# Optimization experiments

Measured on AMD Instinct MI355X. Metric: run time of the kernel, lower is better.

Reference implementation:

```python
import jax, jax.numpy as jnp
import numpy as np

B, TIN, TOUT = 128, 512, 64
IN_F, OUT_F, H = 64, 32, 1024
DEC_IN = IN_F + OUT_F  # decoder GRU input size


def setup_inputs() -> dict:
    key = jax.random.key(0)
    ks = jax.random.split(key, 24)
    s = 1.0 / np.sqrt(H)
    u = lambda k, shp: jax.random.uniform(k, shp, jnp.float32, -s, s)
    return {
        "enc_input": jax.random.normal(ks[0], (B, TIN, IN_F), jnp.float32),
        "dec_input": jax.random.normal(ks[1], (B, TOUT, IN_F), jnp.float32),
        # encoder GRU, layer 0 (input IN_F) and layer 1 (input H); gates stacked [r,z,n]
        "enc_Wih0": u(ks[2], (3 * H, IN_F)), "enc_Whh0": u(ks[3], (3 * H, H)),
        "enc_bih0": u(ks[4], (3 * H,)), "enc_bhh0": u(ks[5], (3 * H,)),
        "enc_Wih1": u(ks[6], (3 * H, H)), "enc_Whh1": u(ks[7], (3 * H, H)),
        "enc_bih1": u(ks[8], (3 * H,)), "enc_bhh1": u(ks[9], (3 * H,)),
        # decoder GRU, layer 0 (input DEC_IN) and layer 1 (input H)
        "dec_Wih0": u(ks[10], (3 * H, DEC_IN)), "dec_Whh0": u(ks[11], (3 * H, H)),
        "dec_bih0": u(ks[12], (3 * H,)), "dec_bhh0": u(ks[13], (3 * H,)),
        "dec_Wih1": u(ks[14], (3 * H, H)), "dec_Whh1": u(ks[15], (3 * H, H)),
        "dec_bih1": u(ks[16], (3 * H,)), "dec_bhh1": u(ks[17], (3 * H,)),
        # output MLP: Linear(H,H)+ReLU, then Linear(H,OUT_F, bias=False)
        "out1_W": u(ks[18], (H, H)), "out1_b": u(ks[19], (H,)),
        "out2_W": u(ks[20], (OUT_F, H)),
    }


def _gru_cell(x, h, Wih, Whh, bih, bhh):
    """Single GRU step, PyTorch gate convention. x:(B,in) h:(B,H) -> (B,H)."""
    gi = x @ Wih.T + bih
    gh = h @ Whh.T + bhh
    ir, iz, inn = jnp.split(gi, 3, axis=-1)
    hr, hz, hn = jnp.split(gh, 3, axis=-1)
    r = jax.nn.sigmoid(ir + hr)
    z = jax.nn.sigmoid(iz + hz)
    n = jnp.tanh(inn + r * hn)
    return (1.0 - z) * n + z * h


def _gru_layer(x, h0, Wih, Whh, bih, bhh):
    """Full-sequence GRU layer. x:(B,T,in) -> (ys:(B,T,H), hT:(B,H))."""
    xp = jnp.einsum('bti,gi->btg', x, Wih) + bih  # precompute input projections
    def step(h, g):
        gh = h @ Whh.T + bhh
        ir, iz, inn = jnp.split(g, 3, axis=-1)
        hr, hz, hn = jnp.split(gh, 3, axis=-1)
        r = jax.nn.sigmoid(ir + hr)
        z = jax.nn.sigmoid(iz + hz)
        n = jnp.tanh(inn + r * hn)
        hnew = (1.0 - z) * n + z * h
        return hnew, hnew
    hT, ys = jax.lax.scan(step, h0, jnp.swapaxes(xp, 0, 1))
    return jnp.swapaxes(ys, 0, 1), hT


def _forward(enc_input, dec_input,
             enc_Wih0, enc_Whh0, enc_bih0, enc_bhh0,
             enc_Wih1, enc_Whh1, enc_bih1, enc_bhh1,
             dec_Wih0, dec_Whh0, dec_bih0, dec_bhh0,
             dec_Wih1, dec_Whh1, dec_bih1, dec_bhh1,
             out1_W, out1_b, out2_W):
    b = enc_input.shape[0]
    zeros = jnp.zeros((b, H), enc_input.dtype)
    # encoder: 2-layer GRU from zero state
    y0, eh0 = _gru_layer(enc_input, zeros, enc_Wih0, enc_Whh0, enc_bih0, enc_bhh0)
    _, eh1 = _gru_layer(y0, zeros, enc_Wih1, enc_Whh1, enc_bih1, enc_bhh1)
    y_prev0 = enc_input[:, -1, :OUT_F]
    def dec_step(carry, x_t):
        y_prev, h0, h1 = carry
        x = jnp.concatenate([y_prev, x_t], axis=-1)  # (B, OUT_F+IN_F)
        h0n = _gru_cell(x, h0, dec_Wih0, dec_Whh0, dec_bih0, dec_bhh0)
        h1n = _gru_cell(h0n, h1, dec_Wih1, dec_Whh1, dec_bih1, dec_bhh1)
        out = jax.nn.relu(h1n @ out1_W.T + out1_b) @ out2_W.T  # dropout=identity (eval)
        return (out, h0n, h1n), out
    _, ys = jax.lax.scan(dec_step, (y_prev0, eh0, eh1), jnp.swapaxes(dec_input, 0, 1))
    return jnp.swapaxes(ys, 0, 1)  # (B, TOUT, OUT_F)


def reference(enc_input, dec_input,
              enc_Wih0, enc_Whh0, enc_bih0, enc_bhh0,
              enc_Wih1, enc_Whh1, enc_bih1, enc_bhh1,
              dec_Wih0, dec_Whh0, dec_bih0, dec_bhh0,
              dec_Wih1, dec_Whh1, dec_bih1, dec_bhh1,
              out1_W, out1_b, out2_W):
    return _forward(enc_input, dec_input,
                    enc_Wih0, enc_Whh0, enc_bih0, enc_bhh0,
                    enc_Wih1, enc_Whh1, enc_bih1, enc_bhh1,
                    dec_Wih0, dec_Whh0, dec_bih0, dec_bhh0,
                    dec_Wih1, dec_Whh1, dec_bih1, dec_bhh1,
                    out1_W, out1_b, out2_W)
```

## Files before the change

### kernel.cpp

```cpp
#include <hip/hip_runtime.h>

typedef unsigned short u16;
typedef __attribute__((ext_vector_type(8))) short bf16x8;
typedef __attribute__((ext_vector_type(4))) float f32x4;

#define Bsz   128
#define TIN   512
#define TOUT  64
#define INF   64
#define OUTF  32
#define Hdim  1024
#define H3    3072

#define K0    1088
#define K1    2048
#define KD0   1120
#define KD1   2048
#define KH    1024

#define SX0  (Bsz * K0)
#define SX1  (Bsz * K1)
#define SXD0 (Bsz * KD0)
#define SXD1 (Bsz * KD1)
#define SH   (Bsz * Hdim)

__device__ __forceinline__ u16 f2bf(float f) {
    union { float f; unsigned u; } c; c.f = f;
    unsigned u = c.u;
    unsigned r = (u + 0x7fffu + ((u >> 16) & 1u)) >> 16;
    return (u16)r;
}

__device__ __forceinline__ f32x4 mfma16(bf16x8 a, bf16x8 b, f32x4 c) {
    return __builtin_amdgcn_mfma_f32_16x16x32_bf16(a, b, c, 0, 0, 0);
}


__global__ void __launch_bounds__(256) pack2(
        const float* __restrict__ A, int KA,
        const float* __restrict__ Bs, int KB,
        u16* __restrict__ dst) {
    int row = blockIdx.y;
    int k = blockIdx.x * 256 + threadIdx.x;
    int K = KA + KB;
    if (k >= K) return;
    float v = (k < KA) ? A[(size_t)row * KA + k] : Bs[(size_t)row * KB + (k - KA)];
    dst[(size_t)row * K + k] = f2bf(v);
}

__global__ void __launch_bounds__(256) pack_bias(
        const float* bi0e, const float* bh0e,
        const float* bi1e, const float* bh1e,
        const float* bi0d, const float* bh0d,
        const float* bi1d, const float* bh1d,
        const float* out1b,
        float* B0, float* B1, float* BD0, float* BD1, float* HB) {
    int j = blockIdx.x * blockDim.x + threadIdx.x;
    if (j >= 1024) return;
    const float* bis[4] = { bi0e, bi1e, bi0d, bi1d };
    const float* bhs[4] = { bh0e, bh1e, bh0d, bh1d };
    float* ds[4] = { B0, B1, BD0, BD1 };
#pragma unroll
    for (int s = 0; s < 4; ++s) {
        ds[s][j]        = bis[s][j]        + bhs[s][j];
        ds[s][1024 + j] = bis[s][1024 + j] + bhs[s][1024 + j];
        ds[s][2048 + j] = bis[s][2048 + j];
        ds[s][3072 + j] = bhs[s][2048 + j];
    }
    HB[j] = out1b[j];
}

__global__ void __launch_bounds__(256) init_state(
        const float* __restrict__ enc_input,
        u16* __restrict__ X0, u16* __restrict__ X1,
        float* __restrict__ H0f, float* __restrict__ H1f) {
    int gtid = blockIdx.x * blockDim.x + threadIdx.x;
    int G = gridDim.x * blockDim.x;
    for (int i = gtid; i < Bsz * Hdim; i += G) { int b = i >> 10, j = i & 1023; X0[(size_t)b * K0 + j] = 0; }
    for (int i = gtid; i < Bsz * INF; i += G) { int b = i >> 6, f = i & 63;
        X0[(size_t)b * K0 + 1024 + f] = f2bf(enc_input[(size_t)b * (TIN * INF) + f]); }
    for (int i = gtid; i < Bsz * Hdim; i += G) { int b = i >> 10, j = i & 1023;
        X1[(size_t)SX1 + (size_t)b * K1 + j] = 0; }
    for (int i = gtid; i < Bsz * Hdim; i += G) { H0f[i] = 0.f; H1f[SH + i] = 0.f; }
}

template <int KB0, int KB1, int SPLIT>
__device__ __forceinline__ void gru_wave(
        const u16* __restrict__ W, const u16* __restrict__ X, int K,
        int j0, int nb0w,
        f32x4& accR, f32x4& accZ, f32x4& accN0, f32x4& accN1) {
    const int lane = threadIdx.x & 63;
    const int l15 = lane & 15, kq = lane >> 4;
    const u16* Wr = W + (size_t)(j0 + l15) * K + kq * 8;
    const u16* Wz = Wr + (size_t)1024 * K;
    const u16* Wn = Wz + (size_t)1024 * K;
    const u16* Xb = X + (size_t)(nb0w + l15) * K + kq * 8;
    accR = (f32x4){0.f, 0.f, 0.f, 0.f};
    accZ = (f32x4){0.f, 0.f, 0.f, 0.f};
    accN0 = (f32x4){0.f, 0.f, 0.f, 0.f};
    accN1 = (f32x4){0.f, 0.f, 0.f, 0.f};
    constexpr int E0 = (SPLIT < KB1) ? SPLIT : KB1;
    constexpr int S1 = (SPLIT > KB0) ? SPLIT : KB0;
#pragma unroll 8
    for (int kb = KB0; kb < E0; ++kb) {
        const int o = kb * 32;
        bf16x8 xb = *(const bf16x8*)(Xb + o);
        accR  = mfma16(*(const bf16x8*)(Wr + o), xb, accR);
        accZ  = mfma16(*(const bf16x8*)(Wz + o), xb, accZ);
        accN0 = mfma16(*(const bf16x8*)(Wn + o), xb, accN0);
    }
#pragma unroll 8
    for (int kb = S1; kb < KB1; ++kb) {
        const int o = kb * 32;
        bf16x8 xb = *(const bf16x8*)(Xb + o);
        accR  = mfma16(*(const bf16x8*)(Wr + o), xb, accR);
        accZ  = mfma16(*(const bf16x8*)(Wz + o), xb, accZ);
        accN1 = mfma16(*(const bf16x8*)(Wn + o), xb, accN1);
    }
}

template <int KBT, int SPLIT>
__device__ __forceinline__ void gru_block(
        const u16* __restrict__ W, const u16* __restrict__ X,
        const float* __restrict__ Hold, const float* __restrict__ Bias,
        int K, int ct, int nb0,
        float* __restrict__ Hnew,
        u16* __restrict__ O1, int ld1, int off1,
        u16* __restrict__ O2, int ld2, int off2,
        float* __restrict__ sred ) {
    const int tid = threadIdx.x, lane = tid & 63, w = tid >> 6;
    const int bg = w & 3, grp = w >> 2;
    const int l15 = lane & 15, kq = lane >> 4;
    const int j0 = ct * 16;
    const int nb0w = nb0 + bg * 16;
    constexpr int MID = KBT / 2;

    f32x4 aR, aZ, aN0, aN1;
    if (grp == 0) gru_wave<0, MID, SPLIT>(W, X, K, j0, nb0w, aR, aZ, aN0, aN1);
    else          gru_wave<MID, KBT, SPLIT>(W, X, K, j0, nb0w, aR, aZ, aN0, aN1);

    float* slot = sred + ((size_t)bg * 64 + lane) * 17;
    if (grp == 1) {
#pragma unroll
        for (int q = 0; q < 4; ++q) {
            slot[q]      = aR[q];
            slot[4 + q]  = aZ[q];
            slot[8 + q]  = aN0[q];
            slot[12 + q] = aN1[q];
        }
    }
    __syncthreads();
    if (grp == 0) {
#pragma unroll
        for (int q = 0; q < 4; ++q) {
            const int j = j0 + kq * 4 + q;
            const int nb = nb0w + l15;
            float R  = aR[q]  + slot[q];
            float Z  = aZ[q]  + slot[4 + q];
            float Nh = aN0[q] + slot[8 + q];
            float Ni = aN1[q] + slot[12 + q];
            float r = 1.f / (1.f + expf(-(R + Bias[j])));
            float z = 1.f / (1.f + expf(-(Z + Bias[1024 + j])));
            float n = tanhf(Ni + Bias[2048 + j] + r * (Nh + Bias[3072 + j]));
            float ho = Hold[(size_t)j * Bsz + nb];
            float hv = (1.f - z) * n + z * ho;
            Hnew[(size_t)j * Bsz + nb] = hv;
            u16 hb = f2bf(hv);
            O1[(size_t)nb * ld1 + off1 + j] = hb;
            if (O2) O2[(size_t)nb * ld2 + off2 + j] = hb;
        }
    }
}

struct KParams {
    const float* enc_input;
    const float* dec_input;
    const u16 *W0, *W1, *WD0, *WD1, *WH1, *WH2;
    const float *B0, *B1, *BD0, *BD1, *HB;
    u16 *X0, *X1, *XD0, *XD1, *Hhead, *Abuf;
    float *H0f, *H1f;
    float* out;
};

__global__ void __launch_bounds__(512, 2) enc_round(KParams p, int r) {
    __shared__ float sred[4 * 64 * 17];
    const int wg = blockIdx.x;
    const int pr = r & 1, pw = pr ^ 1;
    if (wg < 128) {
        if (r < 512) {
            gru_block<34, 32>(p.W0, p.X0 + pr * SX0, p.H0f + pr * SH, p.B0,
                              K0, wg >> 1, (wg & 1) * 64,
                              p.H0f + pw * SH,
                              p.X0 + pw * SX0, K0, 0,
                              p.X1 + pw * SX1, K1, 1024, sred);
            if (r + 1 < 512 && threadIdx.x < 64) {
                int b = wg, f = threadIdx.x;
                p.X0[(size_t)pw * SX0 + (size_t)b * K0 + 1024 + f] =
                    f2bf(p.enc_input[((size_t)b * TIN + (r + 1)) * INF + f]);
            }
        }
    } else {
        if (r >= 1) {
            int w2 = wg - 128;
            gru_block<64, 32>(p.W1, p.X1 + pr * SX1, p.H1f + pr * SH, p.B1,
                              K1, w2 >> 1, (w2 & 1) * 64,
                              p.H1f + pw * SH,
                              p.X1 + pw * SX1, K1, 0,
                              (u16*)nullptr, 0, 0, sred);
        }
    }
}

__global__ void __launch_bounds__(256) transition(KParams p) {
    int gtid = blockIdx.x * 256 + threadIdx.x;
    const int G = 256 * 256;
    for (int i = gtid; i < SH; i += G) p.H1f[i] = p.H1f[SH + i];
    for (int i = gtid; i < Bsz * Hdim; i += G) {
        int b = i >> 10, j = i & 1023;
        p.XD0[(size_t)b * KD0 + j] = p.X0[(size_t)b * K0 + j];
    }
    for (int i = gtid; i < Bsz * OUTF; i += G) {
        int b = i >> 5, f = i & 31;
        p.XD0[(size_t)b * KD0 + 1024 + f] = f2bf(p.enc_input[((size_t)b * TIN + (TIN - 1)) * INF + f]);
    }
    for (int i = gtid; i < Bsz * INF; i += G) {
        int b = i >> 6, f = i & 63;
        p.XD0[(size_t)b * KD0 + 1056 + f] = f2bf(p.dec_input[(size_t)b * (TOUT * INF) + f]);
    }
    for (int i = gtid; i < Bsz * Hdim; i += G) {
        int b = i >> 10, j = i & 1023;
        p.XD1[(size_t)b * KD1 + j] = p.X1[(size_t)SX1 + (size_t)b * K1 + j];
    }
}

__global__ void __launch_bounds__(512, 2) dec_A(KParams p, int t) {
    __shared__ float sred[4 * 64 * 17];
    const int wg = blockIdx.x;
    const int pt = t & 1, pn = pt ^ 1;
    gru_block<35, 32>(p.WD0, p.XD0 + pt * SXD0, p.H0f + pt * SH, p.BD0,
                      KD0, wg >> 1, (wg & 1) * 64,
                      p.H0f + pn * SH,
                      p.XD0 + pn * SXD0, KD0, 0,
                      p.XD1 + pt * SXD1, KD1, 1024, sred);
}

__global__ void __launch_bounds__(512, 2) dec_B(KParams p, int t) {
    __shared__ float sred[4 * 64 * 17];
    const int wg = blockIdx.x;
    const int pt = t & 1, pn = pt ^ 1;
    gru_block<64, 32>(p.WD1, p.XD1 + pt * SXD1, p.H1f + pt * SH, p.BD1,
                      KD1, wg >> 1, (wg & 1) * 64,
                      p.H1f + pn * SH,
                      p.XD1 + pn * SXD1, KD1, 0,
                      p.Hhead, KH, 0, sred);
}

__global__ void __launch_bounds__(256) dec_C(KParams p, int t) {
    const int wg = blockIdx.x;
    const int pn = (t & 1) ^ 1;
    const int tid = threadIdx.x, lane = tid & 63, w = tid >> 6;
    const int l15 = lane & 15, kq = lane >> 4;
    const int ct = wg >> 1, nb0 = (wg & 1) * 64;
    const int j0 = ct * 16;
    const int nb = nb0 + w * 16 + l15;
    const u16* Wr = p.WH1 + (size_t)(j0 + l15) * KH + kq * 8;
    const u16* Xb = p.Hhead + (size_t)nb * KH + kq * 8;
    f32x4 acc = {0.f, 0.f, 0.f, 0.f};
#pragma unroll 8
    for (int kb = 0; kb < KH / 32; ++kb) {
        const int o = kb * 32;
        acc = mfma16(*(const bf16x8*)(Wr + o), *(const bf16x8*)(Xb + o), acc);
    }
#pragma unroll
    for (int q = 0; q < 4; ++q) {
        const int j = j0 + kq * 4 + q;
        float v = acc[q] + p.HB[j];
        v = v > 0.f ? v : 0.f;
        p.Abuf[(size_t)nb * KH + j] = f2bf(v);
    }
    if (t + 1 < TOUT && threadIdx.x < 64) {
        int b = wg, f = threadIdx.x;
        p.XD0[(size_t)pn * SXD0 + (size_t)b * KD0 + 1056 + f] =
            f2bf(p.dec_input[((size_t)b * TOUT + (t + 1)) * INF + f]);
    }
}

__global__ void __launch_bounds__(256) dec_D(KParams p, int t) {
    __shared__ float sred[1024];
    const int wg = blockIdx.x;
    const int pn = (t & 1) ^ 1;
    const int tid = threadIdx.x, lane = tid & 63, w = tid >> 6;
    const int l15 = lane & 15, kq = lane >> 4;
    const int mt = wg & 1, nt = wg >> 1;
    const u16* Wr = p.WH2 + (size_t)(mt * 16 + l15) * KH + kq * 8;
    const u16* Xb = p.Abuf + (size_t)(nt * 16 + l15) * KH + kq * 8;
    f32x4 acc = {0.f, 0.f, 0.f, 0.f};
#pragma unroll 8
    for (int kb = w * 8; kb < w * 8 + 8; ++kb) {
        const int o = kb * 32;
        acc = mfma16(*(const bf16x8*)(Wr + o), *(const bf16x8*)(Xb + o), acc);
    }
#pragma unroll
    for (int q = 0; q < 4; ++q) sred[(w * 64 + lane) * 4 + q] = acc[q];
    __syncthreads();
    if (w == 0) {
#pragma unroll
        for (int q = 0; q < 4; ++q) {
            float s = sred[(0 * 64 + lane) * 4 + q] + sred[(1 * 64 + lane) * 4 + q] +
                      sred[(2 * 64 + lane) * 4 + q] + sred[(3 * 64 + lane) * 4 + q];
            int feat = mt * 16 + kq * 4 + q;
            int b = nt * 16 + l15;
            p.out[(size_t)b * (TOUT * OUTF) + t * OUTF + feat] = s;
            p.XD0[(size_t)pn * SXD0 + (size_t)b * KD0 + 1024 + feat] = f2bf(s);
        }
    }
}

extern "C" void kernel_launch(void* const* d_in, const int* in_sizes, int n_in,
                              void* d_out, int out_size, void* d_ws, size_t ws_size,
                              hipStream_t stream) {
    const float* enc_input = (const float*)d_in[0];
    const float* dec_input = (const float*)d_in[1];
    const float* enc_Wih0 = (const float*)d_in[2];
    const float* enc_Whh0 = (const float*)d_in[3];
    const float* enc_bih0 = (const float*)d_in[4];
    const float* enc_bhh0 = (const float*)d_in[5];
    const float* enc_Wih1 = (const float*)d_in[6];
    const float* enc_Whh1 = (const float*)d_in[7];
    const float* enc_bih1 = (const float*)d_in[8];
    const float* enc_bhh1 = (const float*)d_in[9];
    const float* dec_Wih0 = (const float*)d_in[10];
    const float* dec_Whh0 = (const float*)d_in[11];
    const float* dec_bih0 = (const float*)d_in[12];
    const float* dec_bhh0 = (const float*)d_in[13];
    const float* dec_Wih1 = (const float*)d_in[14];
    const float* dec_Whh1 = (const float*)d_in[15];
    const float* dec_bih1 = (const float*)d_in[16];
    const float* dec_bhh1 = (const float*)d_in[17];
    const float* out1_W = (const float*)d_in[18];
    const float* out1_b = (const float*)d_in[19];
    const float* out2_W = (const float*)d_in[20];

    char* ws = (char*)d_ws;
    size_t off = 0;
    auto alloc = [&](size_t bytes) { size_t o = off; off = (off + bytes + 255) & ~(size_t)255; return o; };

    u16* W0 = (u16*)(ws + alloc((size_t)H3 * K0 * 2));
    u16* W1 = (u16*)(ws + alloc((size_t)H3 * K1 * 2));
    u16* WD0 = (u16*)(ws + alloc((size_t)H3 * KD0 * 2));
    u16* WD1 = (u16*)(ws + alloc((size_t)H3 * KD1 * 2));
    u16* WH1 = (u16*)(ws + alloc((size_t)Hdim * KH * 2));
    u16* WH2 = (u16*)(ws + alloc((size_t)OUTF * KH * 2));
    float* B0 = (float*)(ws + alloc(4096 * 4));
    float* B1 = (float*)(ws + alloc(4096 * 4));
    float* BD0 = (float*)(ws + alloc(4096 * 4));
    float* BD1 = (float*)(ws + alloc(4096 * 4));
    float* HB = (float*)(ws + alloc(1024 * 4));
    u16* X0 = (u16*)(ws + alloc((size_t)2 * Bsz * K0 * 2));
    u16* X1 = (u16*)(ws + alloc((size_t)2 * Bsz * K1 * 2));
    u16* XD0 = (u16*)(ws + alloc((size_t)2 * Bsz * KD0 * 2));
    u16* XD1 = (u16*)(ws + alloc((size_t)2 * Bsz * KD1 * 2));
    float* H0f = (float*)(ws + alloc((size_t)2 * Bsz * Hdim * 4));
    float* H1f = (float*)(ws + alloc((size_t)2 * Bsz * Hdim * 4));
    u16* Hhead = (u16*)(ws + alloc((size_t)Bsz * KH * 2));
    u16* Abuf = (u16*)(ws + alloc((size_t)Bsz * KH * 2));

    pack2<<<dim3((K0 + 255) / 256, H3), 256, 0, stream>>>(enc_Whh0, 1024, enc_Wih0, 64, W0);
    pack2<<<dim3((K1 + 255) / 256, H3), 256, 0, stream>>>(enc_Whh1, 1024, enc_Wih1, 1024, W1);
    pack2<<<dim3((KD0 + 255) / 256, H3), 256, 0, stream>>>(dec_Whh0, 1024, dec_Wih0, 96, WD0);
    pack2<<<dim3((KD1 + 255) / 256, H3), 256, 0, stream>>>(dec_Whh1, 1024, dec_Wih1, 1024, WD1);
    pack2<<<dim3((KH + 255) / 256, Hdim), 256, 0, stream>>>(out1_W, 1024, nullptr, 0, WH1);
    pack2<<<dim3((KH + 255) / 256, OUTF), 256, 0, stream>>>(out2_W, 1024, nullptr, 0, WH2);
    pack_bias<<<4, 256, 0, stream>>>(enc_bih0, enc_bhh0, enc_bih1, enc_bhh1,
                                     dec_bih0, dec_bhh0, dec_bih1, dec_bhh1,
                                     out1_b, B0, B1, BD0, BD1, HB);
    init_state<<<256, 256, 0, stream>>>(enc_input, X0, X1, H0f, H1f);

    KParams kp;
    kp.enc_input = enc_input; kp.dec_input = dec_input;
    kp.W0 = W0; kp.W1 = W1; kp.WD0 = WD0; kp.WD1 = WD1; kp.WH1 = WH1; kp.WH2 = WH2;
    kp.B0 = B0; kp.B1 = B1; kp.BD0 = BD0; kp.BD1 = BD1; kp.HB = HB;
    kp.X0 = X0; kp.X1 = X1; kp.XD0 = XD0; kp.XD1 = XD1; kp.Hhead = Hhead; kp.Abuf = Abuf;
    kp.H0f = H0f; kp.H1f = H1f;
    kp.out = (float*)d_out;

    for (int r = 0; r < 513; ++r)
        enc_round<<<256, 512, 0, stream>>>(kp, r);

    transition<<<256, 256, 0, stream>>>(kp);

    for (int t = 0; t < TOUT; ++t) {
        dec_A<<<128, 512, 0, stream>>>(kp, t);
        dec_B<<<128, 512, 0, stream>>>(kp, t);
        dec_C<<<128, 256, 0, stream>>>(kp, t);
        dec_D<<<16, 256, 0, stream>>>(kp, t);
    }
}
```

Before: 20.66 ms.

## Replace per-step kernel launches with one persistent kernel using hierarchical grid barriers

Merges the 513 encoder rounds, the transition and the 256 decoder sub-kernels into a single persistent kernel of 256 blocks. A two-level atomic grid barrier (leaf counters per 8 blocks, a root counter and a generation word) takes the place of kernel boundaries. The aim is to remove roughly 800 launch gaps and their drain/refill cost. In exchange it depends on all 256 blocks being co-resident, which is not guaranteed by a normal launch. Occupancy drops to 1 block per CU under the new launch bounds, and idle blocks spin in the barrier during the decoder phases.

```diff
diff --git a/kernel.cpp b/kernel.cpp
--- a/kernel.cpp
+++ b/kernel.cpp
@@ -24,6 +24,10 @@
 #define SXD1 (Bsz * KD1)
 #define SH   (Bsz * Hdim)
 
+#define BAR_ROOT 512
+#define BAR_GEN  528
+#define BAR_WORDS 544
+
 __device__ __forceinline__ u16 f2bf(float f) {
     union { float f; unsigned u; } c; c.f = f;
     unsigned u = c.u;
@@ -33,6 +37,28 @@
 
 __device__ __forceinline__ f32x4 mfma16(bf16x8 a, bf16x8 b, f32x4 c) {
     return __builtin_amdgcn_mfma_f32_16x16x32_bf16(a, b, c, 0, 0, 0);
+}
+
+__device__ __forceinline__ void gridbar(unsigned* bar, unsigned target) {
+    __syncthreads();
+    if (threadIdx.x == 0) {
+        __threadfence();
+        unsigned leaf = (blockIdx.x >> 3) << 4;
+        unsigned a = __hip_atomic_fetch_add(&bar[leaf], 1u,
+                        __ATOMIC_RELEASE, __HIP_MEMORY_SCOPE_AGENT);
+        if (((a + 1u) & 7u) == 0u) {
+            unsigned r = __hip_atomic_fetch_add(&bar[BAR_ROOT], 1u,
+                            __ATOMIC_ACQ_REL, __HIP_MEMORY_SCOPE_AGENT);
+            if (((r + 1u) & 31u) == 0u)
+                __hip_atomic_fetch_add(&bar[BAR_GEN], 1u,
+                        __ATOMIC_RELEASE, __HIP_MEMORY_SCOPE_AGENT);
+        }
+        while (__hip_atomic_load(&bar[BAR_GEN],
+                    __ATOMIC_ACQUIRE, __HIP_MEMORY_SCOPE_AGENT) < target)
+            __builtin_amdgcn_s_sleep(2);
+        __threadfence();
+    }
+    __syncthreads();
 }
 
 
@@ -73,9 +99,11 @@
 __global__ void __launch_bounds__(256) init_state(
         const float* __restrict__ enc_input,
         u16* __restrict__ X0, u16* __restrict__ X1,
-        float* __restrict__ H0f, float* __restrict__ H1f) {
+        float* __restrict__ H0f, float* __restrict__ H1f,
+        unsigned* __restrict__ bar) {
     int gtid = blockIdx.x * blockDim.x + threadIdx.x;
     int G = gridDim.x * blockDim.x;
+    for (int i = gtid; i < BAR_WORDS; i += G) bar[i] = 0u;
     for (int i = gtid; i < Bsz * Hdim; i += G) { int b = i >> 10, j = i & 1023; X0[(size_t)b * K0 + j] = 0; }
     for (int i = gtid; i < Bsz * INF; i += G) { int b = i >> 6, f = i & 63;
         X0[(size_t)b * K0 + 1024 + f] = f2bf(enc_input[(size_t)b * (TIN * INF) + f]); }
@@ -180,10 +208,11 @@
     u16 *X0, *X1, *XD0, *XD1, *Hhead, *Abuf;
     float *H0f, *H1f;
     float* out;
+    unsigned* bar;
 };
 
-__global__ void __launch_bounds__(512, 2) enc_round(KParams p, int r) {
-    __shared__ float sred[4 * 64 * 17];
+
+__device__ __forceinline__ void enc_round_body(const KParams& p, int r, float* sred) {
     const int wg = blockIdx.x;
     const int pr = r & 1, pw = pr ^ 1;
     if (wg < 128) {
@@ -211,9 +240,9 @@
     }
 }
 
-__global__ void __launch_bounds__(256) transition(KParams p) {
-    int gtid = blockIdx.x * 256 + threadIdx.x;
-    const int G = 256 * 256;
+__device__ __forceinline__ void transition_body(const KParams& p) {
+    int gtid = blockIdx.x * blockDim.x + threadIdx.x;
+    const int G = 256 * 512;
     for (int i = gtid; i < SH; i += G) p.H1f[i] = p.H1f[SH + i];
     for (int i = gtid; i < Bsz * Hdim; i += G) {
         int b = i >> 10, j = i & 1023;
@@ -233,8 +262,7 @@
     }
 }
 
-__global__ void __launch_bounds__(512, 2) dec_A(KParams p, int t) {
-    __shared__ float sred[4 * 64 * 17];
+__device__ __forceinline__ void dec_A_body(const KParams& p, int t, float* sred) {
     const int wg = blockIdx.x;
     const int pt = t & 1, pn = pt ^ 1;
     gru_block<35, 32>(p.WD0, p.XD0 + pt * SXD0, p.H0f + pt * SH, p.BD0,
@@ -244,8 +272,7 @@
                       p.XD1 + pt * SXD1, KD1, 1024, sred);
 }
 
-__global__ void __launch_bounds__(512, 2) dec_B(KParams p, int t) {
-    __shared__ float sred[4 * 64 * 17];
+__device__ __forceinline__ void dec_B_body(const KParams& p, int t, float* sred) {
     const int wg = blockIdx.x;
     const int pt = t & 1, pn = pt ^ 1;
     gru_block<64, 32>(p.WD1, p.XD1 + pt * SXD1, p.H1f + pt * SH, p.BD1,
@@ -255,53 +282,56 @@
                       p.Hhead, KH, 0, sred);
 }
 
-__global__ void __launch_bounds__(256) dec_C(KParams p, int t) {
+__device__ __forceinline__ void dec_C_body(const KParams& p, int t) {
     const int wg = blockIdx.x;
     const int pn = (t & 1) ^ 1;
     const int tid = threadIdx.x, lane = tid & 63, w = tid >> 6;
-    const int l15 = lane & 15, kq = lane >> 4;
-    const int ct = wg >> 1, nb0 = (wg & 1) * 64;
-    const int j0 = ct * 16;
-    const int nb = nb0 + w * 16 + l15;
-    const u16* Wr = p.WH1 + (size_t)(j0 + l15) * KH + kq * 8;
-    const u16* Xb = p.Hhead + (size_t)nb * KH + kq * 8;
-    f32x4 acc = {0.f, 0.f, 0.f, 0.f};
+    if (w < 4) {
+        const int l15 = lane & 15, kq = lane >> 4;
+        const int ct = wg >> 1, nb0 = (wg & 1) * 64;
+        const int j0 = ct * 16;
+        const int nb = nb0 + w * 16 + l15;
+        const u16* Wr = p.WH1 + (size_t)(j0 + l15) * KH + kq * 8;
+        const u16* Xb = p.Hhead + (size_t)nb * KH + kq * 8;
+        f32x4 acc = {0.f, 0.f, 0.f, 0.f};
 #pragma unroll 8
-    for (int kb = 0; kb < KH / 32; ++kb) {
-        const int o = kb * 32;
-        acc = mfma16(*(const bf16x8*)(Wr + o), *(const bf16x8*)(Xb + o), acc);
-    }
-#pragma unroll
-    for (int q = 0; q < 4; ++q) {
-        const int j = j0 + kq * 4 + q;
-        float v = acc[q] + p.HB[j];
-        v = v > 0.f ? v : 0.f;
-        p.Abuf[(size_t)nb * KH + j] = f2bf(v);
-    }
-    if (t + 1 < TOUT && threadIdx.x < 64) {
-        int b = wg, f = threadIdx.x;
-        p.XD0[(size_t)pn * SXD0 + (size_t)b * KD0 + 1056 + f] =
-            f2bf(p.dec_input[((size_t)b * TOUT + (t + 1)) * INF + f]);
-    }
-}
-
-__global__ void __launch_bounds__(256) dec_D(KParams p, int t) {
-    __shared__ float sred[1024];
+        for (int kb = 0; kb < KH / 32; ++kb) {
+            const int o = kb * 32;
+            acc = mfma16(*(const bf16x8*)(Wr + o), *(const bf16x8*)(Xb + o), acc);
+        }
+#pragma unroll
+        for (int q = 0; q < 4; ++q) {
+            const int j = j0 + kq * 4 + q;
+            float v = acc[q] + p.HB[j];
+            v = v > 0.f ? v : 0.f;
+            p.Abuf[(size_t)nb * KH + j] = f2bf(v);
+        }
+        if (t + 1 < TOUT && tid < 64) {
+            int b = wg, f = tid;
+            p.XD0[(size_t)pn * SXD0 + (size_t)b * KD0 + 1056 + f] =
+                f2bf(p.dec_input[((size_t)b * TOUT + (t + 1)) * INF + f]);
+        }
+    }
+}
+
+__device__ __forceinline__ void dec_D_body(const KParams& p, int t, float* sred) {
     const int wg = blockIdx.x;
     const int pn = (t & 1) ^ 1;
     const int tid = threadIdx.x, lane = tid & 63, w = tid >> 6;
     const int l15 = lane & 15, kq = lane >> 4;
     const int mt = wg & 1, nt = wg >> 1;
-    const u16* Wr = p.WH2 + (size_t)(mt * 16 + l15) * KH + kq * 8;
-    const u16* Xb = p.Abuf + (size_t)(nt * 16 + l15) * KH + kq * 8;
-    f32x4 acc = {0.f, 0.f, 0.f, 0.f};
+    if (w < 4) {
+        const u16* Wr = p.WH2 + (size_t)(mt * 16 + l15) * KH + kq * 8;
+        const u16* Xb = p.Abuf + (size_t)(nt * 16 + l15) * KH + kq * 8;
+        f32x4 acc = {0.f, 0.f, 0.f, 0.f};
 #pragma unroll 8
-    for (int kb = w * 8; kb < w * 8 + 8; ++kb) {
-        const int o = kb * 32;
-        acc = mfma16(*(const bf16x8*)(Wr + o), *(const bf16x8*)(Xb + o), acc);
-    }
-#pragma unroll
-    for (int q = 0; q < 4; ++q) sred[(w * 64 + lane) * 4 + q] = acc[q];
+        for (int kb = w * 8; kb < w * 8 + 8; ++kb) {
+            const int o = kb * 32;
+            acc = mfma16(*(const bf16x8*)(Wr + o), *(const bf16x8*)(Xb + o), acc);
+        }
+#pragma unroll
+        for (int q = 0; q < 4; ++q) sred[(w * 64 + lane) * 4 + q] = acc[q];
+    }
     __syncthreads();
     if (w == 0) {
 #pragma unroll
@@ -313,6 +343,30 @@
             p.out[(size_t)b * (TOUT * OUTF) + t * OUTF + feat] = s;
             p.XD0[(size_t)pn * SXD0 + (size_t)b * KD0 + 1024 + feat] = f2bf(s);
         }
+    }
+}
+
+__global__ void __launch_bounds__(512, 1) seq2seq_persist(KParams p) {
+    __shared__ float sred[4 * 64 * 17];
+    unsigned target = 0;
+
+    for (int r = 0; r < 513; ++r) {
+        enc_round_body(p, r, sred);
+        gridbar(p.bar, ++target);
+    }
+
+    transition_body(p);
+    gridbar(p.bar, ++target);
+
+    for (int t = 0; t < TOUT; ++t) {
+        if (blockIdx.x < 128) dec_A_body(p, t, sred);
+        gridbar(p.bar, ++target);
+        if (blockIdx.x < 128) dec_B_body(p, t, sred);
+        gridbar(p.bar, ++target);
+        if (blockIdx.x < 128) dec_C_body(p, t);
+        gridbar(p.bar, ++target);
+        if (blockIdx.x < 16) dec_D_body(p, t, sred);
+        if (t + 1 < TOUT) gridbar(p.bar, ++target);
     }
 }
 
@@ -364,6 +418,7 @@
     float* H1f = (float*)(ws + alloc((size_t)2 * Bsz * Hdim * 4));
     u16* Hhead = (u16*)(ws + alloc((size_t)Bsz * KH * 2));
     u16* Abuf = (u16*)(ws + alloc((size_t)Bsz * KH * 2));
+    unsigned* bar = (unsigned*)(ws + alloc(BAR_WORDS * 4));
 
     pack2<<<dim3((K0 + 255) / 256, H3), 256, 0, stream>>>(enc_Whh0, 1024, enc_Wih0, 64, W0);
     pack2<<<dim3((K1 + 255) / 256, H3), 256, 0, stream>>>(enc_Whh1, 1024, enc_Wih1, 1024, W1);
@@ -374,7 +429,7 @@
     pack_bias<<<4, 256, 0, stream>>>(enc_bih0, enc_bhh0, enc_bih1, enc_bhh1,
                                      dec_bih0, dec_bhh0, dec_bih1, dec_bhh1,
                                      out1_b, B0, B1, BD0, BD1, HB);
-    init_state<<<256, 256, 0, stream>>>(enc_input, X0, X1, H0f, H1f);
+    init_state<<<256, 256, 0, stream>>>(enc_input, X0, X1, H0f, H1f, bar);
 
     KParams kp;
     kp.enc_input = enc_input; kp.dec_input = dec_input;
@@ -383,16 +438,7 @@
     kp.X0 = X0; kp.X1 = X1; kp.XD0 = XD0; kp.XD1 = XD1; kp.Hhead = Hhead; kp.Abuf = Abuf;
     kp.H0f = H0f; kp.H1f = H1f;
     kp.out = (float*)d_out;
-
-    for (int r = 0; r < 513; ++r)
-        enc_round<<<256, 512, 0, stream>>>(kp, r);
-
-    transition<<<256, 256, 0, stream>>>(kp);
-
-    for (int t = 0; t < TOUT; ++t) {
-        dec_A<<<128, 512, 0, stream>>>(kp, t);
-        dec_B<<<128, 512, 0, stream>>>(kp, t);
-        dec_C<<<128, 256, 0, stream>>>(kp, t);
-        dec_D<<<16, 256, 0, stream>>>(kp, t);
-    }
-}
+    kp.bar = bar;
+
+    seq2seq_persist<<<256, 512, 0, stream>>>(kp);
+}
```

Result: slower. 60.76 ms (+194.1%).
